# Performance work log

Hardware: AMD Instinct MI355X
Metric: run time of the kernel (lower is better)

## Reference

```python
import jax, jax.numpy as jnp
import numpy as np

N_AGENTS = 32
STATE_DIM = 512
EMBED = 64
BATCH = 32768


def setup_inputs() -> dict:
    key = jax.random.key(0)
    ks = jax.random.split(key, 16)
    g = lambda k, shape, fan_in: jax.random.normal(k, shape, jnp.float32) / np.sqrt(fan_in)
    return {
        "agent_qs": jax.random.normal(ks[0], (BATCH, N_AGENTS), jnp.float32),
        "states": jax.random.normal(ks[1], (BATCH, STATE_DIM), jnp.float32),
        # hyper_w1: Linear(state,E) -> ReLU -> Linear(E, n_agents*E)
        "w1_l1_w": g(ks[2], (EMBED, STATE_DIM), STATE_DIM),
        "w1_l1_b": jnp.zeros((EMBED,), jnp.float32),
        "w1_l2_w": g(ks[3], (N_AGENTS * EMBED, EMBED), EMBED),
        "w1_l2_b": jnp.zeros((N_AGENTS * EMBED,), jnp.float32),
        # hyper_w2: Linear(state,E) -> ReLU -> Linear(E, E)
        "w2_l1_w": g(ks[4], (EMBED, STATE_DIM), STATE_DIM),
        "w2_l1_b": jnp.zeros((EMBED,), jnp.float32),
        "w2_l2_w": g(ks[5], (EMBED, EMBED), EMBED),
        "w2_l2_b": jnp.zeros((EMBED,), jnp.float32),
        # hyper_b1: Linear(state, E)
        "b1_w": g(ks[6], (EMBED, STATE_DIM), STATE_DIM),
        "b1_b": jnp.zeros((EMBED,), jnp.float32),
        # hyper_b2: Linear(state,E) -> ReLU -> Linear(E, 1)
        "b2_l1_w": g(ks[7], (EMBED, STATE_DIM), STATE_DIM),
        "b2_l1_b": jnp.zeros((EMBED,), jnp.float32),
        "b2_l2_w": g(ks[8], (1, EMBED), EMBED),
        "b2_l2_b": jnp.zeros((1,), jnp.float32),
    }


def _linear(x, w, b):
    return x @ w.T + b


def reference(agent_qs, states,
              w1_l1_w, w1_l1_b, w1_l2_w, w1_l2_b,
              w2_l1_w, w2_l1_b, w2_l2_w, w2_l2_b,
              b1_w, b1_b, b2_l1_w, b2_l1_b, b2_l2_w, b2_l2_b):
    B = agent_qs.shape[0]
    # hypernetworks producing per-sample weights
    w1 = jnp.abs(_linear(jax.nn.relu(_linear(states, w1_l1_w, w1_l1_b)), w1_l2_w, w1_l2_b))
    w1 = w1.reshape(B, N_AGENTS, EMBED)                      # [B, A, E]
    b1 = _linear(states, b1_w, b1_b)                         # [B, E]
    hidden = jax.nn.elu(jnp.einsum('ba,bae->be', agent_qs, w1) + b1)  # [B, E]
    w2 = jnp.abs(_linear(jax.nn.relu(_linear(states, w2_l1_w, w2_l1_b)), w2_l2_w, w2_l2_b))  # [B, E]
    b2 = _linear(jax.nn.relu(_linear(states, b2_l1_w, b2_l1_b)), b2_l2_w, b2_l2_b)           # [B, 1]
    q_total = jnp.einsum('be,be->b', hidden, w2) + b2[:, 0]  # [B]
    return q_total
```

## Files before the change

kernel.cpp:

```cpp
#include <hip/hip_runtime.h>

typedef unsigned short u16;
typedef unsigned int u32;
typedef short bf16x8 __attribute__((ext_vector_type(8)));
typedef float f32x4 __attribute__((ext_vector_type(4)));
typedef u16 u16x4 __attribute__((ext_vector_type(4)));

#define NAG 32
#define STATE 512
#define EMBED 64
#define TB 64

#define OFF_W1L1 0
#define OFF_W2L1 32768
#define OFF_B1W  65536
#define OFF_B2L1 98304
#define OFF_W1L2 131072
#define OFF_W2L2 262144
#define WS_TOTAL 266240

__device__ __forceinline__ float bf2f(u16 u) {
    u32 i = ((u32)u) << 16; float f;
    __builtin_memcpy(&f, &i, 4); return f;
}
__device__ __forceinline__ u16 f2bf(float f) {
    u32 i; __builtin_memcpy(&i, &f, 4);
    return (u16)((i + 0x8000u) >> 16);
}
__device__ __forceinline__ bf16x8 ld8(const u16* p) {
    return *reinterpret_cast<const bf16x8*>(p);
}
__device__ __forceinline__ bf16x8 cvt8(f32x4 a, f32x4 b) {
    bf16x8 r;
#pragma unroll
    for (int i = 0; i < 4; ++i) r[i]     = (short)f2bf(a[i]);
#pragma unroll
    for (int i = 0; i < 4; ++i) r[i + 4] = (short)f2bf(b[i]);
    return r;
}
__device__ __forceinline__ void dma16(const void* g, void* l) {
    __builtin_amdgcn_global_load_lds(
        (const __attribute__((address_space(1))) u32*)g,
        (__attribute__((address_space(3))) u32*)l, 16, 0, 0);
}

__global__ __launch_bounds__(256) void cvt_weights(
    const float* __restrict__ w1l1w, const float* __restrict__ w2l1w,
    const float* __restrict__ b1w,   const float* __restrict__ b2l1w,
    const float* __restrict__ w1l2w, const float* __restrict__ w2l2w,
    u16* __restrict__ ws)
{
    int idx = blockIdx.x * 256 + threadIdx.x;
    const float* src; int off;
    if      (idx < OFF_W2L1)  { src = w1l1w; off = OFF_W1L1; }
    else if (idx < OFF_B1W)   { src = w2l1w; off = OFF_W2L1; }
    else if (idx < OFF_B2L1)  { src = b1w;   off = OFF_B1W;  }
    else if (idx < OFF_W1L2)  { src = b2l1w; off = OFF_B2L1; }
    else if (idx < OFF_W2L2)  { src = w1l2w; off = OFF_W1L2; }
    else if (idx < WS_TOTAL)  { src = w2l2w; off = OFF_W2L2; }
    else return;
    ws[idx] = f2bf(src[idx - off]);
}

__global__ __launch_bounds__(256, 2) void qmix_kernel(
    const float* __restrict__ qs,    const float* __restrict__ st,
    const u16*  __restrict__ wsb,
    const float* __restrict__ w1l1b, const float* __restrict__ w1l2b,
    const float* __restrict__ w2l1b, const float* __restrict__ w2l2b,
    const float* __restrict__ b1b,   const float* __restrict__ b2l1b,
    const float* __restrict__ b2l2w, const float* __restrict__ b2l2b,
    float* __restrict__ out)
{
    __shared__ u16  wbuf[256 * 64];
    __shared__ u16  y[TB][264];
    __shared__ u16  qslb[TB][40];
    __shared__ u16  w1bs[2048];
    __shared__ float qacc[TB];
    __shared__ float b2wv[64];

    const int t    = threadIdx.x;
    const int wave = t >> 6, lane = t & 63;
    const int m = lane & 15, quad = lane >> 4;
    const int sbase = blockIdx.x * TB;
    const int s0 = wave * 16;

    if (t < 64) b2wv[t] = b2l2w[t];
    {
        f32x4 q0 = *reinterpret_cast<const f32x4*>(qs + (size_t)sbase * NAG + t * 8);
        f32x4 q1 = *reinterpret_cast<const f32x4*>(qs + (size_t)sbase * NAG + t * 8 + 4);
        *reinterpret_cast<bf16x8*>(&qslb[t >> 2][(t & 3) * 8]) = cvt8(q0, q1);
        f32x4 w0 = *reinterpret_cast<const f32x4*>(w1l2b + t * 8);
        f32x4 w1 = *reinterpret_cast<const f32x4*>(w1l2b + t * 8 + 4);
        *reinterpret_cast<bf16x8*>(&w1bs[t * 8]) = cvt8(w0, w1);
    }

    float abias[16];
#pragma unroll
    for (int tt = 0; tt < 4; ++tt) abias[tt]      = w1l1b[tt * 16 + m];
#pragma unroll
    for (int tt = 0; tt < 4; ++tt) abias[tt + 4]  = w2l1b[tt * 16 + m];
#pragma unroll
    for (int tt = 0; tt < 4; ++tt) abias[tt + 8]  = b1b[tt * 16 + m];
#pragma unroll
    for (int tt = 0; tt < 4; ++tt) abias[tt + 12] = b2l1b[tt * 16 + m];

    const float* astB = st + (size_t)(sbase + s0 + m) * STATE + quad * 8;
    const int rsub = lane >> 3, cch = lane & 7;

    f32x4 acc[16] = {};
    for (int ksl = 0; ksl < 8; ++ksl) {
        __syncthreads();
#pragma unroll
        for (int j = 0; j < 8; ++j) {
            const int row = wave * 64 + j * 8 + rsub;
            const int sc  = cch ^ (row & 7);
            dma16(wsb + (size_t)row * STATE + ksl * 64 + sc * 8,
                  &wbuf[(wave * 64 + j * 8) * 64 + lane * 8]);
        }
        f32x4 av0 = *reinterpret_cast<const f32x4*>(astB + ksl * 64);
        f32x4 av1 = *reinterpret_cast<const f32x4*>(astB + ksl * 64 + 4);
        f32x4 av2 = *reinterpret_cast<const f32x4*>(astB + ksl * 64 + 32);
        f32x4 av3 = *reinterpret_cast<const f32x4*>(astB + ksl * 64 + 36);
        __builtin_amdgcn_s_waitcnt(0);
        __syncthreads();
        bf16x8 af0 = cvt8(av0, av1);
        bf16x8 af1 = cvt8(av2, av3);
#pragma unroll
        for (int tt = 0; tt < 16; ++tt) {
            const int brow = tt * 16 + m;
            bf16x8 b0 = ld8(&wbuf[brow * 64 + ((quad) ^ (brow & 7)) * 8]);
            acc[tt] = __builtin_amdgcn_mfma_f32_16x16x32_bf16(af0, b0, acc[tt], 0, 0, 0);
        }
#pragma unroll
        for (int tt = 0; tt < 16; ++tt) {
            const int brow = tt * 16 + m;
            bf16x8 b1 = ld8(&wbuf[brow * 64 + ((4 + quad) ^ (brow & 7)) * 8]);
            acc[tt] = __builtin_amdgcn_mfma_f32_16x16x32_bf16(af1, b1, acc[tt], 0, 0, 0);
        }
    }
#pragma unroll
    for (int tt = 0; tt < 16; ++tt) {
        const bool isrelu = (tt < 8) || (tt >= 12);
        const int fcol = tt * 16 + m;
#pragma unroll
        for (int r = 0; r < 4; ++r) {
            float v = acc[tt][r] + abias[tt];
            if (isrelu) v = fmaxf(v, 0.f);
            y[s0 + quad * 4 + r][fcol] = f2bf(v);
        }
    }
    __syncthreads();

    bf16x8 haf0 = *reinterpret_cast<const bf16x8*>(&y[s0 + m][quad * 8]);
    bf16x8 haf1 = *reinterpret_cast<const bf16x8*>(&y[s0 + m][32 + quad * 8]);

    f32x4 hacc[4] = {};
    for (int bs = 0; bs < 8; ++bs) {
        __syncthreads();
#pragma unroll
        for (int j = 0; j < 8; ++j) {
            const int row = wave * 64 + j * 8 + rsub;
            const int sc  = cch ^ (row & 7);
            dma16(wsb + OFF_W1L2 + ((size_t)bs * 256 + row) * EMBED + sc * 8,
                  &wbuf[(wave * 64 + j * 8) * 64 + lane * 8]);
        }
        u16x4 qv4[4];
#pragma unroll
        for (int r = 0; r < 4; ++r)
            qv4[r] = *reinterpret_cast<const u16x4*>(&qslb[s0 + quad * 4 + r][bs * 4]);
        __builtin_amdgcn_s_waitcnt(0);
        __syncthreads();
#pragma unroll
        for (int aloc = 0; aloc < 4; ++aloc) {
#pragma unroll
            for (int tp = 0; tp < 4; ++tp) {
                const int row = aloc * 64 + tp * 16 + m;
                bf16x8 b0 = ld8(&wbuf[row * 64 + ((quad) ^ (row & 7)) * 8]);
                bf16x8 b1 = ld8(&wbuf[row * 64 + ((4 + quad) ^ (row & 7)) * 8]);
                f32x4 p = {};
                p = __builtin_amdgcn_mfma_f32_16x16x32_bf16(haf0, b0, p, 0, 0, 0);
                p = __builtin_amdgcn_mfma_f32_16x16x32_bf16(haf1, b1, p, 0, 0, 0);
                const float bias = bf2f(w1bs[(bs * 4 + aloc) * EMBED + tp * 16 + m]);
#pragma unroll
                for (int r = 0; r < 4; ++r)
                    hacc[tp][r] += bf2f((u16)qv4[r][aloc]) * fabsf(p[r] + bias);
            }
        }
    }
    __syncthreads();
    u16* hid = wbuf;
#pragma unroll
    for (int tp = 0; tp < 4; ++tp) {
#pragma unroll
        for (int r = 0; r < 4; ++r) {
            const int s = s0 + quad * 4 + r, e = tp * 16 + m;
            float v = hacc[tp][r] + bf2f(y[s][128 + e]);
            v = (v > 0.f) ? v : (__expf(v) - 1.f);
            hid[s * 66 + e] = f2bf(v);
        }
    }
    __syncthreads();

    bf16x8 h2f0 = *reinterpret_cast<const bf16x8*>(&y[s0 + m][64 + quad * 8]);
    bf16x8 h2f1 = *reinterpret_cast<const bf16x8*>(&y[s0 + m][96 + quad * 8]);

    f32x4 qp = {};
#pragma unroll
    for (int tp = 0; tp < 4; ++tp) {
        const u16* wc = wsb + OFF_W2L2 + (size_t)(tp * 16 + m) * EMBED + quad * 8;
        bf16x8 b0 = ld8(wc);
        bf16x8 b1 = ld8(wc + 32);
        f32x4 p = {};
        p = __builtin_amdgcn_mfma_f32_16x16x32_bf16(h2f0, b0, p, 0, 0, 0);
        p = __builtin_amdgcn_mfma_f32_16x16x32_bf16(h2f1, b1, p, 0, 0, 0);
        const float bias = w2l2b[tp * 16 + m];
#pragma unroll
        for (int r = 0; r < 4; ++r)
            qp[r] += bf2f(hid[(s0 + quad * 4 + r) * 66 + tp * 16 + m]) * fabsf(p[r] + bias);
    }
#pragma unroll
    for (int off = 1; off < 16; off <<= 1) {
#pragma unroll
        for (int r = 0; r < 4; ++r) qp[r] += __shfl_xor(qp[r], off, 64);
    }
    if (m == 0) {
#pragma unroll
        for (int r = 0; r < 4; ++r) qacc[s0 + quad * 4 + r] = qp[r];
    }
    __syncthreads();

    if (t < TB) {
        float q = qacc[t] + b2l2b[0];
        float acc2 = 0.f;
#pragma unroll
        for (int kk = 0; kk < 8; ++kk) {
            bf16x8 hv = *reinterpret_cast<const bf16x8*>(&y[t][192 + kk * 8]);
#pragma unroll
            for (int j = 0; j < 8; ++j)
                acc2 += bf2f((u16)hv[j]) * b2wv[kk * 8 + j];
        }
        out[sbase + t] = q + acc2;
    }
}

extern "C" void kernel_launch(void* const* d_in, const int* in_sizes, int n_in,
                              void* d_out, int out_size, void* d_ws, size_t ws_size,
                              hipStream_t stream)
{
    const float* qs    = (const float*)d_in[0];
    const float* st    = (const float*)d_in[1];
    const float* w1l1w = (const float*)d_in[2];
    const float* w1l1b = (const float*)d_in[3];
    const float* w1l2w = (const float*)d_in[4];
    const float* w1l2b = (const float*)d_in[5];
    const float* w2l1w = (const float*)d_in[6];
    const float* w2l1b = (const float*)d_in[7];
    const float* w2l2w = (const float*)d_in[8];
    const float* w2l2b = (const float*)d_in[9];
    const float* b1w   = (const float*)d_in[10];
    const float* b1b   = (const float*)d_in[11];
    const float* b2l1w = (const float*)d_in[12];
    const float* b2l1b = (const float*)d_in[13];
    const float* b2l2w = (const float*)d_in[14];
    const float* b2l2b = (const float*)d_in[15];

    u16* wsb = (u16*)d_ws;

    cvt_weights<<<(WS_TOTAL + 255) / 256, 256, 0, stream>>>(
        w1l1w, w2l1w, b1w, b2l1w, w1l2w, w2l2w, wsb);

    int B = in_sizes[0] / NAG;
    int grid = B / TB;
    qmix_kernel<<<grid, 256, 0, stream>>>(
        qs, st, wsb,
        w1l1b, w1l2b, w2l1b, w2l2b, b1b, b2l1b, b2l2w, b2l2b,
        (float*)d_out);
}
```

Before: 152.1 us.

## Double samples per block so each wave reuses weight tiles across two row groups

Raises the block tile from 64 to 128 samples, so each wave computes two 16-row groups against every weight fragment it loads from LDS. K slices for the first GEMM widen to 128, and the w1 second-layer chunks widen to 512 rows, which halves the number of staging rounds and barriers. The intent is to halve global and LDS weight traffic per sample and cut synchronisation overhead. In exchange, shared memory roughly doubles and launch bounds drop to one block per CU, which reduces latency hiding and leaves about one block per CU for the whole grid.

```diff
diff --git a/kernel.cpp b/kernel.cpp
--- a/kernel.cpp
+++ b/kernel.cpp
@@ -4,12 +4,11 @@
 typedef unsigned int u32;
 typedef short bf16x8 __attribute__((ext_vector_type(8)));
 typedef float f32x4 __attribute__((ext_vector_type(4)));
-typedef u16 u16x4 __attribute__((ext_vector_type(4)));
 
 #define NAG 32
 #define STATE 512
 #define EMBED 64
-#define TB 64
+#define TB 128
 
 #define OFF_W1L1 0
 #define OFF_W2L1 32768
@@ -62,7 +61,7 @@
     ws[idx] = f2bf(src[idx - off]);
 }
 
-__global__ __launch_bounds__(256, 2) void qmix_kernel(
+__global__ __launch_bounds__(256, 1) void qmix_kernel(
     const float* __restrict__ qs,    const float* __restrict__ st,
     const u16*  __restrict__ wsb,
     const float* __restrict__ w1l1b, const float* __restrict__ w1l2b,
@@ -71,7 +70,7 @@
     const float* __restrict__ b2l2w, const float* __restrict__ b2l2b,
     float* __restrict__ out)
 {
-    __shared__ u16  wbuf[256 * 64];
+    __shared__ u16  wbuf[32768];
     __shared__ u16  y[TB][264];
     __shared__ u16  qslb[TB][40];
     __shared__ u16  w1bs[2048];
@@ -82,13 +81,18 @@
     const int wave = t >> 6, lane = t & 63;
     const int m = lane & 15, quad = lane >> 4;
     const int sbase = blockIdx.x * TB;
-    const int s0 = wave * 16;
+    const int s0 = wave * 32;
 
     if (t < 64) b2wv[t] = b2l2w[t];
     {
-        f32x4 q0 = *reinterpret_cast<const f32x4*>(qs + (size_t)sbase * NAG + t * 8);
-        f32x4 q1 = *reinterpret_cast<const f32x4*>(qs + (size_t)sbase * NAG + t * 8 + 4);
-        *reinterpret_cast<bf16x8*>(&qslb[t >> 2][(t & 3) * 8]) = cvt8(q0, q1);
+        const int r = t >> 1, h = t & 1;
+        const float* qp0 = qs + (size_t)(sbase + r) * NAG + h * 16;
+        f32x4 q0 = *reinterpret_cast<const f32x4*>(qp0);
+        f32x4 q1 = *reinterpret_cast<const f32x4*>(qp0 + 4);
+        f32x4 q2 = *reinterpret_cast<const f32x4*>(qp0 + 8);
+        f32x4 q3 = *reinterpret_cast<const f32x4*>(qp0 + 12);
+        *reinterpret_cast<bf16x8*>(&qslb[r][h * 16])     = cvt8(q0, q1);
+        *reinterpret_cast<bf16x8*>(&qslb[r][h * 16 + 8]) = cvt8(q2, q3);
         f32x4 w0 = *reinterpret_cast<const f32x4*>(w1l2b + t * 8);
         f32x4 w1 = *reinterpret_cast<const f32x4*>(w1l2b + t * 8 + 4);
         *reinterpret_cast<bf16x8*>(&w1bs[t * 8]) = cvt8(w0, w1);
@@ -104,38 +108,43 @@
 #pragma unroll
     for (int tt = 0; tt < 4; ++tt) abias[tt + 12] = b2l1b[tt * 16 + m];
 
-    const float* astB = st + (size_t)(sbase + s0 + m) * STATE + quad * 8;
-    const int rsub = lane >> 3, cch = lane & 7;
-
-    f32x4 acc[16] = {};
-    for (int ksl = 0; ksl < 8; ++ksl) {
+    const float* sp0 = st + (size_t)(sbase + s0 + m) * STATE;
+    const int r4 = lane >> 4, c16 = lane & 15;
+    const int r8 = lane >> 3, c8 = lane & 7;
+
+    f32x4 acc0[16] = {}, acc1[16] = {};
+    for (int ksl = 0; ksl < 4; ++ksl) {
         __syncthreads();
 #pragma unroll
-        for (int j = 0; j < 8; ++j) {
-            const int row = wave * 64 + j * 8 + rsub;
-            const int sc  = cch ^ (row & 7);
-            dma16(wsb + (size_t)row * STATE + ksl * 64 + sc * 8,
-                  &wbuf[(wave * 64 + j * 8) * 64 + lane * 8]);
-        }
-        f32x4 av0 = *reinterpret_cast<const f32x4*>(astB + ksl * 64);
-        f32x4 av1 = *reinterpret_cast<const f32x4*>(astB + ksl * 64 + 4);
-        f32x4 av2 = *reinterpret_cast<const f32x4*>(astB + ksl * 64 + 32);
-        f32x4 av3 = *reinterpret_cast<const f32x4*>(astB + ksl * 64 + 36);
+        for (int j = 0; j < 16; ++j) {
+            const int row = wave * 64 + j * 4 + r4;
+            const int sc  = c16 ^ (row & 15);
+            dma16(wsb + (size_t)row * STATE + ksl * 128 + sc * 8,
+                  &wbuf[(wave * 64 + j * 4) * 128 + lane * 8]);
+        }
+        f32x4 av[2][4][2];
+#pragma unroll
+        for (int g = 0; g < 2; ++g)
+#pragma unroll
+            for (int ks = 0; ks < 4; ++ks) {
+                const float* p = sp0 + g * 16 * STATE + ksl * 128 + ks * 32 + quad * 8;
+                av[g][ks][0] = *reinterpret_cast<const f32x4*>(p);
+                av[g][ks][1] = *reinterpret_cast<const f32x4*>(p + 4);
+            }
         __builtin_amdgcn_s_waitcnt(0);
         __syncthreads();
-        bf16x8 af0 = cvt8(av0, av1);
-        bf16x8 af1 = cvt8(av2, av3);
-#pragma unroll
-        for (int tt = 0; tt < 16; ++tt) {
-            const int brow = tt * 16 + m;
-            bf16x8 b0 = ld8(&wbuf[brow * 64 + ((quad) ^ (brow & 7)) * 8]);
-            acc[tt] = __builtin_amdgcn_mfma_f32_16x16x32_bf16(af0, b0, acc[tt], 0, 0, 0);
-        }
-#pragma unroll
-        for (int tt = 0; tt < 16; ++tt) {
-            const int brow = tt * 16 + m;
-            bf16x8 b1 = ld8(&wbuf[brow * 64 + ((4 + quad) ^ (brow & 7)) * 8]);
-            acc[tt] = __builtin_amdgcn_mfma_f32_16x16x32_bf16(af1, b1, acc[tt], 0, 0, 0);
+#pragma unroll
+        for (int ks = 0; ks < 4; ++ks) {
+            bf16x8 af0 = cvt8(av[0][ks][0], av[0][ks][1]);
+            bf16x8 af1 = cvt8(av[1][ks][0], av[1][ks][1]);
+#pragma unroll
+            for (int tt = 0; tt < 16; ++tt) {
+                const int row = tt * 16 + m;
+                const int lc = (ks * 4 + quad) ^ (row & 15);
+                bf16x8 b = ld8(&wbuf[row * 128 + lc * 8]);
+                acc0[tt] = __builtin_amdgcn_mfma_f32_16x16x32_bf16(af0, b, acc0[tt], 0, 0, 0);
+                acc1[tt] = __builtin_amdgcn_mfma_f32_16x16x32_bf16(af1, b, acc1[tt], 0, 0, 0);
+            }
         }
     }
 #pragma unroll
@@ -144,88 +153,112 @@
         const int fcol = tt * 16 + m;
 #pragma unroll
         for (int r = 0; r < 4; ++r) {
-            float v = acc[tt][r] + abias[tt];
-            if (isrelu) v = fmaxf(v, 0.f);
-            y[s0 + quad * 4 + r][fcol] = f2bf(v);
+            float v0 = acc0[tt][r] + abias[tt];
+            float v1 = acc1[tt][r] + abias[tt];
+            if (isrelu) { v0 = fmaxf(v0, 0.f); v1 = fmaxf(v1, 0.f); }
+            y[s0 + quad * 4 + r][fcol]      = f2bf(v0);
+            y[s0 + 16 + quad * 4 + r][fcol] = f2bf(v1);
         }
     }
     __syncthreads();
 
-    bf16x8 haf0 = *reinterpret_cast<const bf16x8*>(&y[s0 + m][quad * 8]);
-    bf16x8 haf1 = *reinterpret_cast<const bf16x8*>(&y[s0 + m][32 + quad * 8]);
-
-    f32x4 hacc[4] = {};
-    for (int bs = 0; bs < 8; ++bs) {
+    bf16x8 haf[2][2];
+#pragma unroll
+    for (int g = 0; g < 2; ++g) {
+        haf[g][0] = *reinterpret_cast<const bf16x8*>(&y[s0 + g * 16 + m][quad * 8]);
+        haf[g][1] = *reinterpret_cast<const bf16x8*>(&y[s0 + g * 16 + m][32 + quad * 8]);
+    }
+
+    f32x4 hacc[2][4] = {};
+    for (int bs = 0; bs < 4; ++bs) {
         __syncthreads();
 #pragma unroll
-        for (int j = 0; j < 8; ++j) {
-            const int row = wave * 64 + j * 8 + rsub;
-            const int sc  = cch ^ (row & 7);
-            dma16(wsb + OFF_W1L2 + ((size_t)bs * 256 + row) * EMBED + sc * 8,
-                  &wbuf[(wave * 64 + j * 8) * 64 + lane * 8]);
-        }
-        u16x4 qv4[4];
-#pragma unroll
-        for (int r = 0; r < 4; ++r)
-            qv4[r] = *reinterpret_cast<const u16x4*>(&qslb[s0 + quad * 4 + r][bs * 4]);
+        for (int j = 0; j < 16; ++j) {
+            const int row = wave * 128 + j * 8 + r8;
+            const int sc  = c8 ^ (row & 7);
+            dma16(wsb + OFF_W1L2 + ((size_t)bs * 512 + row) * EMBED + sc * 8,
+                  &wbuf[(wave * 128 + j * 8) * 64 + lane * 8]);
+        }
+        bf16x8 qv8[2][4];
+#pragma unroll
+        for (int g = 0; g < 2; ++g)
+#pragma unroll
+            for (int r = 0; r < 4; ++r)
+                qv8[g][r] = *reinterpret_cast<const bf16x8*>(&qslb[s0 + g * 16 + quad * 4 + r][bs * 8]);
         __builtin_amdgcn_s_waitcnt(0);
         __syncthreads();
 #pragma unroll
-        for (int aloc = 0; aloc < 4; ++aloc) {
+        for (int aloc = 0; aloc < 8; ++aloc) {
 #pragma unroll
             for (int tp = 0; tp < 4; ++tp) {
                 const int row = aloc * 64 + tp * 16 + m;
                 bf16x8 b0 = ld8(&wbuf[row * 64 + ((quad) ^ (row & 7)) * 8]);
                 bf16x8 b1 = ld8(&wbuf[row * 64 + ((4 + quad) ^ (row & 7)) * 8]);
-                f32x4 p = {};
-                p = __builtin_amdgcn_mfma_f32_16x16x32_bf16(haf0, b0, p, 0, 0, 0);
-                p = __builtin_amdgcn_mfma_f32_16x16x32_bf16(haf1, b1, p, 0, 0, 0);
-                const float bias = bf2f(w1bs[(bs * 4 + aloc) * EMBED + tp * 16 + m]);
-#pragma unroll
-                for (int r = 0; r < 4; ++r)
-                    hacc[tp][r] += bf2f((u16)qv4[r][aloc]) * fabsf(p[r] + bias);
+                const float bias = bf2f(w1bs[(bs * 8 + aloc) * EMBED + tp * 16 + m]);
+#pragma unroll
+                for (int g = 0; g < 2; ++g) {
+                    f32x4 p = {};
+                    p = __builtin_amdgcn_mfma_f32_16x16x32_bf16(haf[g][0], b0, p, 0, 0, 0);
+                    p = __builtin_amdgcn_mfma_f32_16x16x32_bf16(haf[g][1], b1, p, 0, 0, 0);
+#pragma unroll
+                    for (int r = 0; r < 4; ++r)
+                        hacc[g][tp][r] += bf2f((u16)qv8[g][r][aloc]) * fabsf(p[r] + bias);
+                }
             }
         }
     }
     __syncthreads();
     u16* hid = wbuf;
 #pragma unroll
-    for (int tp = 0; tp < 4; ++tp) {
-#pragma unroll
-        for (int r = 0; r < 4; ++r) {
-            const int s = s0 + quad * 4 + r, e = tp * 16 + m;
-            float v = hacc[tp][r] + bf2f(y[s][128 + e]);
-            v = (v > 0.f) ? v : (__expf(v) - 1.f);
-            hid[s * 66 + e] = f2bf(v);
-        }
-    }
+    for (int g = 0; g < 2; ++g)
+#pragma unroll
+        for (int tp = 0; tp < 4; ++tp)
+#pragma unroll
+            for (int r = 0; r < 4; ++r) {
+                const int s = s0 + g * 16 + quad * 4 + r, e = tp * 16 + m;
+                float v = hacc[g][tp][r] + bf2f(y[s][128 + e]);
+                v = (v > 0.f) ? v : (__expf(v) - 1.f);
+                hid[s * 66 + e] = f2bf(v);
+            }
     __syncthreads();
 
-    bf16x8 h2f0 = *reinterpret_cast<const bf16x8*>(&y[s0 + m][64 + quad * 8]);
-    bf16x8 h2f1 = *reinterpret_cast<const bf16x8*>(&y[s0 + m][96 + quad * 8]);
-
-    f32x4 qp = {};
+    bf16x8 h2f[2][2];
+#pragma unroll
+    for (int g = 0; g < 2; ++g) {
+        h2f[g][0] = *reinterpret_cast<const bf16x8*>(&y[s0 + g * 16 + m][64 + quad * 8]);
+        h2f[g][1] = *reinterpret_cast<const bf16x8*>(&y[s0 + g * 16 + m][96 + quad * 8]);
+    }
+
+    f32x4 qp[2] = {};
 #pragma unroll
     for (int tp = 0; tp < 4; ++tp) {
         const u16* wc = wsb + OFF_W2L2 + (size_t)(tp * 16 + m) * EMBED + quad * 8;
         bf16x8 b0 = ld8(wc);
         bf16x8 b1 = ld8(wc + 32);
-        f32x4 p = {};
-        p = __builtin_amdgcn_mfma_f32_16x16x32_bf16(h2f0, b0, p, 0, 0, 0);
-        p = __builtin_amdgcn_mfma_f32_16x16x32_bf16(h2f1, b1, p, 0, 0, 0);
         const float bias = w2l2b[tp * 16 + m];
 #pragma unroll
-        for (int r = 0; r < 4; ++r)
-            qp[r] += bf2f(hid[(s0 + quad * 4 + r) * 66 + tp * 16 + m]) * fabsf(p[r] + bias);
+        for (int g = 0; g < 2; ++g) {
+            f32x4 p = {};
+            p = __builtin_amdgcn_mfma_f32_16x16x32_bf16(h2f[g][0], b0, p, 0, 0, 0);
+            p = __builtin_amdgcn_mfma_f32_16x16x32_bf16(h2f[g][1], b1, p, 0, 0, 0);
+#pragma unroll
+            for (int r = 0; r < 4; ++r)
+                qp[g][r] += bf2f(hid[(s0 + g * 16 + quad * 4 + r) * 66 + tp * 16 + m])
+                            * fabsf(p[r] + bias);
+        }
     }
 #pragma unroll
     for (int off = 1; off < 16; off <<= 1) {
 #pragma unroll
-        for (int r = 0; r < 4; ++r) qp[r] += __shfl_xor(qp[r], off, 64);
+        for (int g = 0; g < 2; ++g)
+#pragma unroll
+            for (int r = 0; r < 4; ++r) qp[g][r] += __shfl_xor(qp[g][r], off, 64);
     }
     if (m == 0) {
 #pragma unroll
-        for (int r = 0; r < 4; ++r) qacc[s0 + quad * 4 + r] = qp[r];
+        for (int g = 0; g < 2; ++g)
+#pragma unroll
+            for (int r = 0; r < 4; ++r) qacc[s0 + g * 16 + quad * 4 + r] = qp[g][r];
     }
     __syncthreads();
 
```

New measurement: 163.0 us. 1.07x slower.

## Halve batch tile and split waves across features to raise occupancy

Applied to the files above, without the earlier changes.

Cuts the per-block sample tile from 64 to 32 and reassigns the four waves as 2 sample-halves × 2 feature-halves, so each wave holds 8 instead of 16 accumulator tiles in the first GEMM and 2 instead of 4 in the mixing stage. The staged weight slices shrink (32-wide K slices, 128-row W1L2 chunks) with a new swizzle, halving LDS, and launch bounds move from 2 to 4 blocks per CU. The final reduction combines two per-wave partial sums. The cost is twice as many blocks each re-streaming the full weight set, and twice as many K/chunk iterations with a barrier each, in exchange for more resident waves to hide latency.

```diff
diff --git a/kernel.cpp b/kernel.cpp
--- a/kernel.cpp
+++ b/kernel.cpp
@@ -4,12 +4,11 @@
 typedef unsigned int u32;
 typedef short bf16x8 __attribute__((ext_vector_type(8)));
 typedef float f32x4 __attribute__((ext_vector_type(4)));
-typedef u16 u16x4 __attribute__((ext_vector_type(4)));
 
 #define NAG 32
 #define STATE 512
 #define EMBED 64
-#define TB 64
+#define TB 32
 
 #define OFF_W1L1 0
 #define OFF_W2L1 32768
@@ -62,7 +61,7 @@
     ws[idx] = f2bf(src[idx - off]);
 }
 
-__global__ __launch_bounds__(256, 2) void qmix_kernel(
+__global__ __launch_bounds__(256, 4) void qmix_kernel(
     const float* __restrict__ qs,    const float* __restrict__ st,
     const u16*  __restrict__ wsb,
     const float* __restrict__ w1l1b, const float* __restrict__ w1l2b,
@@ -71,77 +70,75 @@
     const float* __restrict__ b2l2w, const float* __restrict__ b2l2b,
     float* __restrict__ out)
 {
-    __shared__ u16  wbuf[256 * 64];
+    __shared__ u16  wbuf[8192];
     __shared__ u16  y[TB][264];
     __shared__ u16  qslb[TB][40];
     __shared__ u16  w1bs[2048];
-    __shared__ float qacc[TB];
+    __shared__ float qacc[TB][2];
     __shared__ float b2wv[64];
 
     const int t    = threadIdx.x;
     const int wave = t >> 6, lane = t & 63;
     const int m = lane & 15, quad = lane >> 4;
     const int sbase = blockIdx.x * TB;
-    const int s0 = wave * 16;
 
     if (t < 64) b2wv[t] = b2l2w[t];
+    if (t < 128) {
+        const int r = t >> 2, h = t & 3;
+        const float* qp0 = qs + (size_t)(sbase + r) * NAG + h * 8;
+        f32x4 q0 = *reinterpret_cast<const f32x4*>(qp0);
+        f32x4 q1 = *reinterpret_cast<const f32x4*>(qp0 + 4);
+        *reinterpret_cast<bf16x8*>(&qslb[r][h * 8]) = cvt8(q0, q1);
+    }
     {
-        f32x4 q0 = *reinterpret_cast<const f32x4*>(qs + (size_t)sbase * NAG + t * 8);
-        f32x4 q1 = *reinterpret_cast<const f32x4*>(qs + (size_t)sbase * NAG + t * 8 + 4);
-        *reinterpret_cast<bf16x8*>(&qslb[t >> 2][(t & 3) * 8]) = cvt8(q0, q1);
         f32x4 w0 = *reinterpret_cast<const f32x4*>(w1l2b + t * 8);
         f32x4 w1 = *reinterpret_cast<const f32x4*>(w1l2b + t * 8 + 4);
         *reinterpret_cast<bf16x8*>(&w1bs[t * 8]) = cvt8(w0, w1);
     }
 
-    float abias[16];
-#pragma unroll
-    for (int tt = 0; tt < 4; ++tt) abias[tt]      = w1l1b[tt * 16 + m];
-#pragma unroll
-    for (int tt = 0; tt < 4; ++tt) abias[tt + 4]  = w2l1b[tt * 16 + m];
-#pragma unroll
-    for (int tt = 0; tt < 4; ++tt) abias[tt + 8]  = b1b[tt * 16 + m];
-#pragma unroll
-    for (int tt = 0; tt < 4; ++tt) abias[tt + 12] = b2l1b[tt * 16 + m];
-
-    const float* astB = st + (size_t)(sbase + s0 + m) * STATE + quad * 8;
-    const int rsub = lane >> 3, cch = lane & 7;
-
-    f32x4 acc[16] = {};
-    for (int ksl = 0; ksl < 8; ++ksl) {
-        __syncthreads();
-#pragma unroll
-        for (int j = 0; j < 8; ++j) {
-            const int row = wave * 64 + j * 8 + rsub;
-            const int sc  = cch ^ (row & 7);
-            dma16(wsb + (size_t)row * STATE + ksl * 64 + sc * 8,
-                  &wbuf[(wave * 64 + j * 8) * 64 + lane * 8]);
-        }
-        f32x4 av0 = *reinterpret_cast<const f32x4*>(astB + ksl * 64);
-        f32x4 av1 = *reinterpret_cast<const f32x4*>(astB + ksl * 64 + 4);
-        f32x4 av2 = *reinterpret_cast<const f32x4*>(astB + ksl * 64 + 32);
-        f32x4 av3 = *reinterpret_cast<const f32x4*>(astB + ksl * 64 + 36);
+    const int shalf = wave >> 1, fhalf = wave & 1;
+    const int s0 = shalf * 16;
+    const int fbase = fhalf * 128;
+
+    const float* bgA = fhalf ? b1b   : w1l1b;
+    const float* bgB = fhalf ? b2l1b : w2l1b;
+    float abias[8];
+#pragma unroll
+    for (int tt = 0; tt < 4; ++tt) abias[tt]     = bgA[tt * 16 + m];
+#pragma unroll
+    for (int tt = 0; tt < 4; ++tt) abias[tt + 4] = bgB[tt * 16 + m];
+
+    const float* sp0 = st + (size_t)(sbase + s0 + m) * STATE + quad * 8;
+    const int rA = lane >> 2, cA = lane & 3;
+    const int rB = lane >> 3, cB = lane & 7;
+
+    f32x4 acc[8] = {};
+    for (int ksl = 0; ksl < 16; ++ksl) {
+        __syncthreads();
+#pragma unroll
+        for (int j = 0; j < 4; ++j) {
+            const int row = wave * 64 + j * 16 + rA;
+            const int sc  = cA ^ (row & 3) ^ ((row >> 2) & 3);
+            dma16(wsb + (size_t)row * STATE + ksl * 32 + sc * 8,
+                  &wbuf[(wave * 64 + j * 16) * 32 + lane * 8]);
+        }
+        f32x4 av0 = *reinterpret_cast<const f32x4*>(sp0 + ksl * 32);
+        f32x4 av1 = *reinterpret_cast<const f32x4*>(sp0 + ksl * 32 + 4);
         __builtin_amdgcn_s_waitcnt(0);
         __syncthreads();
-        bf16x8 af0 = cvt8(av0, av1);
-        bf16x8 af1 = cvt8(av2, av3);
-#pragma unroll
-        for (int tt = 0; tt < 16; ++tt) {
-            const int brow = tt * 16 + m;
-            bf16x8 b0 = ld8(&wbuf[brow * 64 + ((quad) ^ (brow & 7)) * 8]);
-            acc[tt] = __builtin_amdgcn_mfma_f32_16x16x32_bf16(af0, b0, acc[tt], 0, 0, 0);
-        }
-#pragma unroll
-        for (int tt = 0; tt < 16; ++tt) {
-            const int brow = tt * 16 + m;
-            bf16x8 b1 = ld8(&wbuf[brow * 64 + ((4 + quad) ^ (brow & 7)) * 8]);
-            acc[tt] = __builtin_amdgcn_mfma_f32_16x16x32_bf16(af1, b1, acc[tt], 0, 0, 0);
-        }
-    }
-#pragma unroll
-    for (int tt = 0; tt < 16; ++tt) {
-        const bool isrelu = (tt < 8) || (tt >= 12);
-        const int fcol = tt * 16 + m;
+        bf16x8 af = cvt8(av0, av1);
+#pragma unroll
+        for (int tt = 0; tt < 8; ++tt) {
+            const int row = fbase + tt * 16 + m;
+            const int lc  = quad ^ (row & 3) ^ ((row >> 2) & 3);
+            bf16x8 b = ld8(&wbuf[row * 32 + lc * 8]);
+            acc[tt] = __builtin_amdgcn_mfma_f32_16x16x32_bf16(af, b, acc[tt], 0, 0, 0);
+        }
+    }
+#pragma unroll
+    for (int tt = 0; tt < 8; ++tt) {
+        const bool isrelu = (fhalf == 0) || (tt >= 4);
+        const int fcol = fbase + tt * 16 + m;
 #pragma unroll
         for (int r = 0; r < 4; ++r) {
             float v = acc[tt][r] + abias[tt];
@@ -151,49 +148,50 @@
     }
     __syncthreads();
 
+    const int e0 = (wave & 1) * 32;
     bf16x8 haf0 = *reinterpret_cast<const bf16x8*>(&y[s0 + m][quad * 8]);
     bf16x8 haf1 = *reinterpret_cast<const bf16x8*>(&y[s0 + m][32 + quad * 8]);
 
-    f32x4 hacc[4] = {};
-    for (int bs = 0; bs < 8; ++bs) {
-        __syncthreads();
-#pragma unroll
-        for (int j = 0; j < 8; ++j) {
-            const int row = wave * 64 + j * 8 + rsub;
-            const int sc  = cch ^ (row & 7);
-            dma16(wsb + OFF_W1L2 + ((size_t)bs * 256 + row) * EMBED + sc * 8,
-                  &wbuf[(wave * 64 + j * 8) * 64 + lane * 8]);
-        }
-        u16x4 qv4[4];
-#pragma unroll
-        for (int r = 0; r < 4; ++r)
-            qv4[r] = *reinterpret_cast<const u16x4*>(&qslb[s0 + quad * 4 + r][bs * 4]);
+    f32x4 hacc[2] = {};
+    for (int bs = 0; bs < 16; ++bs) {
+        __syncthreads();
+#pragma unroll
+        for (int j = 0; j < 4; ++j) {
+            const int row = wave * 32 + j * 8 + rB;
+            const int sc  = cB ^ (row & 7);
+            dma16(wsb + OFF_W1L2 + ((size_t)bs * 128 + row) * EMBED + sc * 8,
+                  &wbuf[(wave * 32 + j * 8) * 64 + lane * 8]);
+        }
         __builtin_amdgcn_s_waitcnt(0);
         __syncthreads();
 #pragma unroll
-        for (int aloc = 0; aloc < 4; ++aloc) {
-#pragma unroll
-            for (int tp = 0; tp < 4; ++tp) {
-                const int row = aloc * 64 + tp * 16 + m;
+        for (int aloc = 0; aloc < 2; ++aloc) {
+            float qv[4];
+#pragma unroll
+            for (int r = 0; r < 4; ++r)
+                qv[r] = bf2f(qslb[s0 + quad * 4 + r][bs * 2 + aloc]);
+#pragma unroll
+            for (int tp = 0; tp < 2; ++tp) {
+                const int row = aloc * 64 + e0 + tp * 16 + m;
                 bf16x8 b0 = ld8(&wbuf[row * 64 + ((quad) ^ (row & 7)) * 8]);
                 bf16x8 b1 = ld8(&wbuf[row * 64 + ((4 + quad) ^ (row & 7)) * 8]);
                 f32x4 p = {};
                 p = __builtin_amdgcn_mfma_f32_16x16x32_bf16(haf0, b0, p, 0, 0, 0);
                 p = __builtin_amdgcn_mfma_f32_16x16x32_bf16(haf1, b1, p, 0, 0, 0);
-                const float bias = bf2f(w1bs[(bs * 4 + aloc) * EMBED + tp * 16 + m]);
+                const float bias = bf2f(w1bs[(bs * 2 + aloc) * EMBED + e0 + tp * 16 + m]);
 #pragma unroll
                 for (int r = 0; r < 4; ++r)
-                    hacc[tp][r] += bf2f((u16)qv4[r][aloc]) * fabsf(p[r] + bias);
+                    hacc[tp][r] += qv[r] * fabsf(p[r] + bias);
             }
         }
     }
     __syncthreads();
     u16* hid = wbuf;
 #pragma unroll
-    for (int tp = 0; tp < 4; ++tp) {
+    for (int tp = 0; tp < 2; ++tp) {
 #pragma unroll
         for (int r = 0; r < 4; ++r) {
-            const int s = s0 + quad * 4 + r, e = tp * 16 + m;
+            const int s = s0 + quad * 4 + r, e = e0 + tp * 16 + m;
             float v = hacc[tp][r] + bf2f(y[s][128 + e]);
             v = (v > 0.f) ? v : (__expf(v) - 1.f);
             hid[s * 66 + e] = f2bf(v);
@@ -206,17 +204,18 @@
 
     f32x4 qp = {};
 #pragma unroll
-    for (int tp = 0; tp < 4; ++tp) {
-        const u16* wc = wsb + OFF_W2L2 + (size_t)(tp * 16 + m) * EMBED + quad * 8;
+    for (int tp = 0; tp < 2; ++tp) {
+        const int etile = (wave & 1) * 2 + tp;
+        const u16* wc = wsb + OFF_W2L2 + (size_t)(etile * 16 + m) * EMBED + quad * 8;
         bf16x8 b0 = ld8(wc);
         bf16x8 b1 = ld8(wc + 32);
         f32x4 p = {};
         p = __builtin_amdgcn_mfma_f32_16x16x32_bf16(h2f0, b0, p, 0, 0, 0);
         p = __builtin_amdgcn_mfma_f32_16x16x32_bf16(h2f1, b1, p, 0, 0, 0);
-        const float bias = w2l2b[tp * 16 + m];
+        const float bias = w2l2b[etile * 16 + m];
 #pragma unroll
         for (int r = 0; r < 4; ++r)
-            qp[r] += bf2f(hid[(s0 + quad * 4 + r) * 66 + tp * 16 + m]) * fabsf(p[r] + bias);
+            qp[r] += bf2f(hid[(s0 + quad * 4 + r) * 66 + etile * 16 + m]) * fabsf(p[r] + bias);
     }
 #pragma unroll
     for (int off = 1; off < 16; off <<= 1) {
@@ -225,12 +224,12 @@
     }
     if (m == 0) {
 #pragma unroll
-        for (int r = 0; r < 4; ++r) qacc[s0 + quad * 4 + r] = qp[r];
+        for (int r = 0; r < 4; ++r) qacc[s0 + quad * 4 + r][wave & 1] = qp[r];
     }
     __syncthreads();
 
     if (t < TB) {
-        float q = qacc[t] + b2l2b[0];
+        float q = qacc[t][0] + qacc[t][1] + b2l2b[0];
         float acc2 = 0.f;
 #pragma unroll
         for (int kk = 0; kk < 8; ++kk) {
```

Result: slower. 173.5 us (+14.1%).

## Double-buffer weight staging and repartition w1 stage by embed column per wave

Applied to the files above, without the earlier changes.

Replaces the single LDS weight buffer with two buffers and prefetches the next K-slice (and the first w1_l2 slice during the last state slice) while computing the current one. Global-to-LDS waits use partial vmcnt instead of a full drain. The weight layout becomes chunk-major so it needs no swizzle. The per-agent w1 stage is repartitioned so each wave owns 16 embed columns across all 64 samples, which reuses each staged weight fragment across four sample groups. To support that, the agent Qs are transposed into LDS. The aim is to hide global load latency behind MFMA work and halve the LDS footprint per stage, at the cost of more barriers (16 steps instead of 8) and uncoalesced scalar reads of qs.

```diff
diff --git a/kernel.cpp b/kernel.cpp
--- a/kernel.cpp
+++ b/kernel.cpp
@@ -43,6 +43,29 @@
         (const __attribute__((address_space(1))) u32*)g,
         (__attribute__((address_space(3))) u32*)l, 16, 0, 0);
 }
+
+#define VMW(n) __builtin_amdgcn_s_waitcnt(0x0F70 | (n))
+#define BARRIER() asm volatile("s_barrier" ::: "memory")
+
+#define STAGE_A(ksl, buf) do {                                          \
+    const u16* _s = wsb + (size_t)(wave * 64 + lane) * STATE + (ksl) * 32; \
+    u16* _d = &wa[buf][(wave * 64 + lane) * 8];                         \
+    dma16(_s,      _d);                                                 \
+    dma16(_s + 8,  _d + 2048);                                          \
+    dma16(_s + 16, _d + 4096);                                          \
+    dma16(_s + 24, _d + 6144);                                          \
+} while (0)
+
+#define STAGE_B(bs, buf) do {                                           \
+    _Pragma("unroll")                                                   \
+    for (int _j = 0; _j < 4; ++_j) {                                    \
+        const int _idx = wave * 4 + _j;                                 \
+        const int _c = _idx >> 1, _h = _idx & 1;                        \
+        const int _r = _h * 64 + lane;                                  \
+        dma16(wsb + OFF_W1L2 + ((size_t)(bs) * 128 + _r) * EMBED + _c * 8, \
+              &wa[buf][(_c * 128 + _r) * 8]);                           \
+    }                                                                   \
+} while (0)
 
 __global__ __launch_bounds__(256) void cvt_weights(
     const float* __restrict__ w1l1w, const float* __restrict__ w2l1w,
@@ -71,9 +94,9 @@
     const float* __restrict__ b2l2w, const float* __restrict__ b2l2b,
     float* __restrict__ out)
 {
-    __shared__ u16  wbuf[256 * 64];
+    __shared__ u16  wa[2][8192];
     __shared__ u16  y[TB][264];
-    __shared__ u16  qslb[TB][40];
+    __shared__ u16  qsT[NAG][72];
     __shared__ u16  w1bs[2048];
     __shared__ float qacc[TB];
     __shared__ float b2wv[64];
@@ -86,14 +109,16 @@
 
     if (t < 64) b2wv[t] = b2l2w[t];
     {
-        f32x4 q0 = *reinterpret_cast<const f32x4*>(qs + (size_t)sbase * NAG + t * 8);
-        f32x4 q1 = *reinterpret_cast<const f32x4*>(qs + (size_t)sbase * NAG + t * 8 + 4);
-        *reinterpret_cast<bf16x8*>(&qslb[t >> 2][(t & 3) * 8]) = cvt8(q0, q1);
         f32x4 w0 = *reinterpret_cast<const f32x4*>(w1l2b + t * 8);
         f32x4 w1 = *reinterpret_cast<const f32x4*>(w1l2b + t * 8 + 4);
         *reinterpret_cast<bf16x8*>(&w1bs[t * 8]) = cvt8(w0, w1);
     }
-
+    {
+        const int a = t & 31, sg = (t >> 5) * 8;
+#pragma unroll
+        for (int k = 0; k < 8; ++k)
+            qsT[a][sg + k] = f2bf(qs[(size_t)(sbase + sg + k) * NAG + a]);
+    }
     float abias[16];
 #pragma unroll
     for (int tt = 0; tt < 4; ++tt) abias[tt]      = w1l1b[tt * 16 + m];
@@ -104,39 +129,34 @@
 #pragma unroll
     for (int tt = 0; tt < 4; ++tt) abias[tt + 12] = b2l1b[tt * 16 + m];
 
-    const float* astB = st + (size_t)(sbase + s0 + m) * STATE + quad * 8;
-    const int rsub = lane >> 3, cch = lane & 7;
+    const float* sp0 = st + (size_t)(sbase + s0 + m) * STATE + quad * 8;
+    f32x4 sa0 = *reinterpret_cast<const f32x4*>(sp0);
+    f32x4 sb0 = *reinterpret_cast<const f32x4*>(sp0 + 4);
+    STAGE_A(0, 0);
 
     f32x4 acc[16] = {};
-    for (int ksl = 0; ksl < 8; ++ksl) {
-        __syncthreads();
-#pragma unroll
-        for (int j = 0; j < 8; ++j) {
-            const int row = wave * 64 + j * 8 + rsub;
-            const int sc  = cch ^ (row & 7);
-            dma16(wsb + (size_t)row * STATE + ksl * 64 + sc * 8,
-                  &wbuf[(wave * 64 + j * 8) * 64 + lane * 8]);
-        }
-        f32x4 av0 = *reinterpret_cast<const f32x4*>(astB + ksl * 64);
-        f32x4 av1 = *reinterpret_cast<const f32x4*>(astB + ksl * 64 + 4);
-        f32x4 av2 = *reinterpret_cast<const f32x4*>(astB + ksl * 64 + 32);
-        f32x4 av3 = *reinterpret_cast<const f32x4*>(astB + ksl * 64 + 36);
-        __builtin_amdgcn_s_waitcnt(0);
-        __syncthreads();
-        bf16x8 af0 = cvt8(av0, av1);
-        bf16x8 af1 = cvt8(av2, av3);
+    f32x4 sa1, sb1;
+    for (int s = 0; s < 16; ++s) {
+        BARRIER();
+        if (s < 15) {
+            STAGE_A(s + 1, (s + 1) & 1);
+            sa1 = *reinterpret_cast<const f32x4*>(sp0 + (s + 1) * 32);
+            sb1 = *reinterpret_cast<const f32x4*>(sp0 + (s + 1) * 32 + 4);
+            VMW(6);
+        } else {
+            STAGE_B(0, 0);
+            VMW(4);
+        }
+        BARRIER();
+        bf16x8 af = cvt8(sa0, sb0);
+        const u16* wb = wa[s & 1];
 #pragma unroll
         for (int tt = 0; tt < 16; ++tt) {
-            const int brow = tt * 16 + m;
-            bf16x8 b0 = ld8(&wbuf[brow * 64 + ((quad) ^ (brow & 7)) * 8]);
-            acc[tt] = __builtin_amdgcn_mfma_f32_16x16x32_bf16(af0, b0, acc[tt], 0, 0, 0);
-        }
-#pragma unroll
-        for (int tt = 0; tt < 16; ++tt) {
-            const int brow = tt * 16 + m;
-            bf16x8 b1 = ld8(&wbuf[brow * 64 + ((4 + quad) ^ (brow & 7)) * 8]);
-            acc[tt] = __builtin_amdgcn_mfma_f32_16x16x32_bf16(af1, b1, acc[tt], 0, 0, 0);
-        }
+            const int row = tt * 16 + m;
+            bf16x8 b = ld8(&wb[(quad * 256 + row) * 8]);
+            acc[tt] = __builtin_amdgcn_mfma_f32_16x16x32_bf16(af, b, acc[tt], 0, 0, 0);
+        }
+        sa0 = sa1; sb0 = sb1;
     }
 #pragma unroll
     for (int tt = 0; tt < 16; ++tt) {
@@ -151,54 +171,55 @@
     }
     __syncthreads();
 
-    bf16x8 haf0 = *reinterpret_cast<const bf16x8*>(&y[s0 + m][quad * 8]);
-    bf16x8 haf1 = *reinterpret_cast<const bf16x8*>(&y[s0 + m][32 + quad * 8]);
+    const int e = wave * 16 + m;
+    bf16x8 haf[4][2];
+#pragma unroll
+    for (int g = 0; g < 4; ++g) {
+        haf[g][0] = *reinterpret_cast<const bf16x8*>(&y[g * 16 + m][quad * 8]);
+        haf[g][1] = *reinterpret_cast<const bf16x8*>(&y[g * 16 + m][32 + quad * 8]);
+    }
 
     f32x4 hacc[4] = {};
-    for (int bs = 0; bs < 8; ++bs) {
-        __syncthreads();
-#pragma unroll
-        for (int j = 0; j < 8; ++j) {
-            const int row = wave * 64 + j * 8 + rsub;
-            const int sc  = cch ^ (row & 7);
-            dma16(wsb + OFF_W1L2 + ((size_t)bs * 256 + row) * EMBED + sc * 8,
-                  &wbuf[(wave * 64 + j * 8) * 64 + lane * 8]);
-        }
-        u16x4 qv4[4];
-#pragma unroll
-        for (int r = 0; r < 4; ++r)
-            qv4[r] = *reinterpret_cast<const u16x4*>(&qslb[s0 + quad * 4 + r][bs * 4]);
-        __builtin_amdgcn_s_waitcnt(0);
-        __syncthreads();
-#pragma unroll
-        for (int aloc = 0; aloc < 4; ++aloc) {
-#pragma unroll
-            for (int tp = 0; tp < 4; ++tp) {
-                const int row = aloc * 64 + tp * 16 + m;
-                bf16x8 b0 = ld8(&wbuf[row * 64 + ((quad) ^ (row & 7)) * 8]);
-                bf16x8 b1 = ld8(&wbuf[row * 64 + ((4 + quad) ^ (row & 7)) * 8]);
+    for (int bs = 0; bs < 16; ++bs) {
+        BARRIER();
+        if (bs < 15) {
+            STAGE_B(bs + 1, (bs + 1) & 1);
+            VMW(4);
+        } else {
+            VMW(0);
+        }
+        BARRIER();
+        const u16* wb = wa[bs & 1];
+#pragma unroll
+        for (int aloc = 0; aloc < 2; ++aloc) {
+            const int row = aloc * 64 + wave * 16 + m;
+            bf16x8 b0 = ld8(&wb[(quad * 128 + row) * 8]);
+            bf16x8 b1 = ld8(&wb[((4 + quad) * 128 + row) * 8]);
+            const int a = bs * 2 + aloc;
+            const float bias = bf2f(w1bs[a * EMBED + e]);
+#pragma unroll
+            for (int g = 0; g < 4; ++g) {
                 f32x4 p = {};
-                p = __builtin_amdgcn_mfma_f32_16x16x32_bf16(haf0, b0, p, 0, 0, 0);
-                p = __builtin_amdgcn_mfma_f32_16x16x32_bf16(haf1, b1, p, 0, 0, 0);
-                const float bias = bf2f(w1bs[(bs * 4 + aloc) * EMBED + tp * 16 + m]);
+                p = __builtin_amdgcn_mfma_f32_16x16x32_bf16(haf[g][0], b0, p, 0, 0, 0);
+                p = __builtin_amdgcn_mfma_f32_16x16x32_bf16(haf[g][1], b1, p, 0, 0, 0);
+                u16x4 qv = *reinterpret_cast<const u16x4*>(&qsT[a][g * 16 + quad * 4]);
 #pragma unroll
                 for (int r = 0; r < 4; ++r)
-                    hacc[tp][r] += bf2f((u16)qv4[r][aloc]) * fabsf(p[r] + bias);
+                    hacc[g][r] += bf2f((u16)qv[r]) * fabsf(p[r] + bias);
             }
         }
     }
     __syncthreads();
-    u16* hid = wbuf;
-#pragma unroll
-    for (int tp = 0; tp < 4; ++tp) {
+    u16* hid = (u16*)wa;
+#pragma unroll
+    for (int g = 0; g < 4; ++g)
 #pragma unroll
         for (int r = 0; r < 4; ++r) {
-            const int s = s0 + quad * 4 + r, e = tp * 16 + m;
-            float v = hacc[tp][r] + bf2f(y[s][128 + e]);
+            const int s = g * 16 + quad * 4 + r;
+            float v = hacc[g][r] + bf2f(y[s][128 + e]);
             v = (v > 0.f) ? v : (__expf(v) - 1.f);
             hid[s * 66 + e] = f2bf(v);
         }
-    }
     __syncthreads();
 
     bf16x8 h2f0 = *reinterpret_cast<const bf16x8*>(&y[s0 + m][64 + quad * 8]);
```

After: 169.9 us. +11.7%, slower.
